# Optimization experiments

Measured on AMD Instinct MI355X. Metric: run time of the kernel, lower is better.

Reference implementation:

```python
import jax, jax.numpy as jnp
import numpy as np

N, E = 50000, 800000
IN_C, HID, OUT_C = 100, 128, 40
LAYERS, GROUPS, CODES = 3, 3, 16
BETA = 0.98
EPS = 1e-5


def setup_inputs() -> dict:
    key = jax.random.key(0)
    ks = jax.random.split(key, 16)
    lin = lambda k, i, o: (jax.random.normal(k, (i, o), jnp.float32) / np.sqrt(i)).astype(jnp.float32)
    d = {}
    d["x"] = jax.random.normal(ks[0], (N, IN_C), jnp.float32)
    d["src"] = jax.random.randint(ks[1], (E,), 0, N, jnp.int32)
    d["dst"] = jax.random.randint(ks[2], (E,), 0, N, jnp.int32)
    # SAGEConv params: lin_l (aggregated, with bias) and lin_r (root, no bias)
    d["W0a"], d["W0r"], d["b0"] = lin(ks[3], IN_C, HID), lin(ks[4], IN_C, HID), jnp.zeros((HID,), jnp.float32)
    d["W1a"], d["W1r"], d["b1"] = lin(ks[5], HID, HID), lin(ks[6], HID, HID), jnp.zeros((HID,), jnp.float32)
    d["W2a"], d["W2r"], d["b2"] = lin(ks[7], HID, HID), lin(ks[8], HID, HID), jnp.zeros((HID,), jnp.float32)
    # BatchNorm (eval mode: running stats) for first num_layers-1 = 2 layers
    d["bn_gamma"] = jnp.ones((2, HID), jnp.float32)
    d["bn_beta"] = jnp.zeros((2, HID), jnp.float32)
    d["bn_mean"] = jnp.zeros((2, HID), jnp.float32)
    d["bn_var"] = jnp.ones((2, HID), jnp.float32)
    # Residual VQ codebooks: [layer, group, num_codes, feature]
    d["codebooks"] = 0.1 * jax.random.normal(ks[9], (LAYERS, GROUPS, CODES, HID), jnp.float32)
    d["lin_W"] = lin(ks[10], HID, OUT_C)
    d["lin_b"] = jnp.zeros((OUT_C,), jnp.float32)
    return d


def _sage_conv(h, src, dst, Wa, Wr, b):
    # mean neighbor aggregation (PyG SAGEConv, aggr='mean')
    msg = h[src]                                              # [E, d]
    agg = jax.ops.segment_sum(msg, dst, num_segments=N)       # [N, d]
    deg = jax.ops.segment_sum(jnp.ones((E,), h.dtype), dst, num_segments=N)
    agg = agg / jnp.maximum(deg, 1.0)[:, None]
    return agg @ Wa + b + h @ Wr


def _rvq(h, cb):
    # residual vector quantization over GROUPS codebooks; cb: [G, K, D]
    res, quant, ids = h, jnp.zeros_like(h), []
    for g in range(GROUPS):
        c = cb[g]                                             # [K, D]
        d2 = (jnp.sum(res * res, -1, keepdims=True)
              - 2.0 * res @ c.T + jnp.sum(c * c, -1))          # [N, K]
        idx = jnp.argmin(d2, axis=-1)
        q = c[idx]
        quant = quant + q
        res = res - q
        ids.append(idx)
    sg = jax.lax.stop_gradient
    loss = (BETA * jnp.mean((h - sg(quant)) ** 2)
            + (1.0 - BETA) * jnp.mean((sg(h) - quant) ** 2))
    return loss, jnp.stack(ids, axis=1)                        # [N, G] int


def reference(x, src, dst, W0a, W0r, b0, W1a, W1r, b1, W2a, W2r, b2,
              bn_gamma, bn_beta, bn_mean, bn_var, codebooks, lin_W, lin_b):
    Ws = [(W0a, W0r, b0), (W1a, W1r, b1), (W2a, W2r, b2)]
    h = x
    total_loss = jnp.float32(0.0)
    id_list = []
    for i in range(LAYERS - 1):
        h = _sage_conv(h, src, dst, *Ws[i])
        h = (h - bn_mean[i]) * jax.lax.rsqrt(bn_var[i] + EPS) * bn_gamma[i] + bn_beta[i]
        h = jax.nn.relu(h)                                     # dropout: eval mode (identity)
        loss, ids = _rvq(h, codebooks[i])
        total_loss = total_loss + loss
        id_list.append(ids)
    h = _sage_conv(h, src, dst, *Ws[-1])
    loss, ids = _rvq(h, codebooks[-1])
    total_loss = total_loss + loss
    id_list.append(ids)
    out = h @ lin_W + lin_b
    return out, total_loss, jnp.concatenate(id_list, axis=1)
```

## Files before the change

### kernel.cpp

```cpp
#include <hip/hip_runtime.h>

#define NN 50000
#define HID 128
#define IN_C 100
#define OUT_C 40

__global__ __launch_bounds__(256)
void hist_kernel(const int* __restrict__ dst, int* __restrict__ deg, int E) {
    int e = blockIdx.x * 256 + threadIdx.x;
    if (e < E) atomicAdd(&deg[dst[e]], 1);
}

__global__ __launch_bounds__(256)
void chunk_sum_kernel(const int* __restrict__ deg, int* __restrict__ chunk_sums, int N) {
    __shared__ int s[256];
    const int t = threadIdx.x;
    const int i = blockIdx.x * 256 + t;
    s[t] = (i < N) ? deg[i] : 0;
    __syncthreads();
    for (int o = 128; o; o >>= 1) { if (t < o) s[t] += s[t + o]; __syncthreads(); }
    if (t == 0) chunk_sums[blockIdx.x] = s[0];
}

__global__ __launch_bounds__(256)
void chunk_scan_kernel(int* __restrict__ chunk_sums, int M) {
    __shared__ int s[256];
    const int t = threadIdx.x;
    int v = (t < M) ? chunk_sums[t] : 0;
    s[t] = v;
    __syncthreads();
    for (int o = 1; o < 256; o <<= 1) {
        int x = (t >= o) ? s[t - o] : 0;
        __syncthreads();
        s[t] += x;
        __syncthreads();
    }
    if (t < M) chunk_sums[t] = s[t] - v;
}

__global__ __launch_bounds__(256)
void chunk_apply_kernel(const int* __restrict__ deg, const int* __restrict__ chunk_sums,
                        int* __restrict__ row_start, int* __restrict__ cursor, int N) {
    __shared__ int s[256];
    const int t = threadIdx.x;
    const int i = blockIdx.x * 256 + t;
    int v = (i < N) ? deg[i] : 0;
    s[t] = v;
    __syncthreads();
    for (int o = 1; o < 256; o <<= 1) {
        int x = (t >= o) ? s[t - o] : 0;
        __syncthreads();
        s[t] += x;
        __syncthreads();
    }
    if (i < N) {
        int ex = chunk_sums[blockIdx.x] + s[t] - v;
        row_start[i] = ex;
        cursor[i] = ex;
        if (i == N - 1) row_start[N] = ex + v;
    }
}

__global__ __launch_bounds__(256)
void scatter_kernel(const int* __restrict__ src, const int* __restrict__ dst,
                    int* __restrict__ cursor, int* __restrict__ csr_src, int E) {
    int e = blockIdx.x * 256 + threadIdx.x;
    if (e < E) {
        int pos = atomicAdd(&cursor[dst[e]], 1);
        csr_src[pos] = src[e];
    }
}

__device__ __forceinline__ double2 ld2(const double* p) {
    return *(const double2*)p;
}
__device__ __forceinline__ double2 ld2(const float* p) {
    float2 v = *(const float2*)p;
    return make_double2((double)v.x, (double)v.y);
}

template<int K, bool HAS_BN, bool LAST, typename TIN>
__global__ __launch_bounds__(512, 6)
void layer_fused(const TIN* __restrict__ h_in,
                 const int* __restrict__ row_start, const int* __restrict__ csr_src,
                 const float* __restrict__ Wa, const float* __restrict__ Wr,
                 const float* __restrict__ b,
                 const float* __restrict__ gamma, const float* __restrict__ beta,
                 const float* __restrict__ mean, const float* __restrict__ var,
                 const float* __restrict__ cb,
                 double* __restrict__ h_out,
                 float* __restrict__ ids_out, int id_col0,
                 double* __restrict__ loss_part,
                 const float* __restrict__ lin_W, const float* __restrict__ lin_b,
                 float* __restrict__ out) {
    __shared__ double s_agg[8][HID];
    __shared__ double s_h[8][HID];
    __shared__ float s_cb[3 * 16 * HID];
    const int t = threadIdx.x;
    const int w = t >> 6, lane = t & 63;
    const int n0 = blockIdx.x * 8;

    for (int idx = t; idx < 3 * 16 * HID; idx += 512) s_cb[idx] = cb[idx];

    {
        const int n = n0 + w;
        const int r0 = row_start[n], r1 = row_start[n + 1];
        const int f0 = 2 * lane;
        if (f0 < K) {
            double s0 = 0, s1 = 0, s2 = 0, s3 = 0, s4 = 0, s5 = 0, s6 = 0, s7 = 0;
            int i = r0;
            for (; i + 3 < r1; i += 4) {
                double2 v0 = ld2(h_in + (size_t)csr_src[i] * K + f0);
                double2 v1 = ld2(h_in + (size_t)csr_src[i + 1] * K + f0);
                double2 v2 = ld2(h_in + (size_t)csr_src[i + 2] * K + f0);
                double2 v3 = ld2(h_in + (size_t)csr_src[i + 3] * K + f0);
                s0 += v0.x; s1 += v0.y; s2 += v1.x; s3 += v1.y;
                s4 += v2.x; s5 += v2.y; s6 += v3.x; s7 += v3.y;
            }
            for (; i < r1; ++i) {
                double2 v = ld2(h_in + (size_t)csr_src[i] * K + f0);
                s0 += v.x; s1 += v.y;
            }
            const int deg = r1 - r0;
            const double dd = (double)(deg > 1 ? deg : 1);
            const double2 root = ld2(h_in + (size_t)n * K + f0);
            s_agg[w][f0]     = ((s0 + s2) + (s4 + s6)) / dd;
            s_agg[w][f0 + 1] = ((s1 + s3) + (s5 + s7)) / dd;
            s_h[w][f0]     = root.x;
            s_h[w][f0 + 1] = root.y;
        }
    }
    __syncthreads();

    const int col = t & 127;
    const int p4 = t >> 7;
    double accA = (double)b[col];
    double accB = accA;
#pragma unroll 4
    for (int k = 0; k < K; ++k) {
        const double wa = (double)Wa[(size_t)k * HID + col];
        const double wr = (double)Wr[(size_t)k * HID + col];
        accA += s_agg[p4][k] * wa + s_h[p4][k] * wr;
        accB += s_agg[p4 + 4][k] * wa + s_h[p4 + 4][k] * wr;
    }
    __syncthreads();

    {
        double vA = accA, vB = accB;
        if (HAS_BN) {
            const double scale = (double)gamma[col] / sqrt((double)var[col] + 1e-5);
            const double shift = (double)beta[col] - (double)mean[col] * scale;
            vA = vA * scale + shift; vA = vA > 0.0 ? vA : 0.0;
            vB = vB * scale + shift; vB = vB > 0.0 ? vB : 0.0;
        }
        h_out[(size_t)(n0 + p4) * HID + col] = vA;
        h_out[(size_t)(n0 + p4 + 4) * HID + col] = vB;
        s_agg[p4][col] = vA;
        s_agg[p4 + 4][col] = vB;
        if (LAST) {
            s_h[p4][col] = vA;
            s_h[p4 + 4][col] = vB;
        }
    }
    __syncthreads();

    double wl;
    {
        double* res = &s_agg[w][0];
        const int n = n0 + w;
        const int k = lane & 15, q = lane >> 4;
        const int jbase = q * 32;
        const int rot = (k + 8 * q) & 31;

        for (int g = 0; g < 3; ++g) {
            const float* c = &s_cb[(g * 16 + k) * HID];
            double r0 = res[lane], r1 = res[lane + 64];
            double pr = r0 * r0 + r1 * r1;
            pr += __shfl_xor(pr, 1, 64);
            pr += __shfl_xor(pr, 2, 64);
            pr += __shfl_xor(pr, 4, 64);
            pr += __shfl_xor(pr, 8, 64);
            pr += __shfl_xor(pr, 16, 64);
            pr += __shfl_xor(pr, 32, 64);
            const float rr32 = (float)pr;

            double cc = 0.0, dot = 0.0;
#pragma unroll
            for (int j2 = 0; j2 < 32; ++j2) {
                const int j = jbase + ((j2 + rot) & 31);
                const double cj = (double)c[j];
                cc += cj * cj;
                dot += res[j] * cj;
            }
            cc += __shfl_xor(cc, 16, 64);
            cc += __shfl_xor(cc, 32, 64);
            dot += __shfl_xor(dot, 16, 64);
            dot += __shfl_xor(dot, 32, 64);

            const float cc32 = (float)cc;
            const float rc32 = (float)dot;
            const float t1 = rr32 - 2.0f * rc32;
            const float d2 = t1 + cc32;

            float bv = d2; int bk = k;
            {
                float ov; int ok;
                ov = __shfl_xor(bv, 1, 64); ok = __shfl_xor(bk, 1, 64);
                if (ov < bv || (ov == bv && ok < bk)) { bv = ov; bk = ok; }
                ov = __shfl_xor(bv, 2, 64); ok = __shfl_xor(bk, 2, 64);
                if (ov < bv || (ov == bv && ok < bk)) { bv = ov; bk = ok; }
                ov = __shfl_xor(bv, 4, 64); ok = __shfl_xor(bk, 4, 64);
                if (ov < bv || (ov == bv && ok < bk)) { bv = ov; bk = ok; }
                ov = __shfl_xor(bv, 8, 64); ok = __shfl_xor(bk, 8, 64);
                if (ov < bv || (ov == bv && ok < bk)) { bv = ov; bk = ok; }
            }
            if (lane == 0)
                ids_out[(size_t)n * 9 + id_col0 + g] = (float)bk;

            const float* cbest = &s_cb[(g * 16 + bk) * HID];
            res[lane]      -= (double)cbest[lane];
            res[lane + 64] -= (double)cbest[lane + 64];
        }
        double r0 = res[lane], r1 = res[lane + 64];
        wl = r0 * r0 + r1 * r1;
        wl += __shfl_xor(wl, 1, 64);
        wl += __shfl_xor(wl, 2, 64);
        wl += __shfl_xor(wl, 4, 64);
        wl += __shfl_xor(wl, 8, 64);
        wl += __shfl_xor(wl, 16, 64);
        wl += __shfl_xor(wl, 32, 64);
    }

    __syncthreads();
    if (lane == 0) s_agg[0][w] = wl;

    if (LAST) {
        const int n = n0 + w;
        if (lane < OUT_C) {
            double acc = (double)lin_b[lane];
            for (int kk = 0; kk < HID; ++kk)
                acc += s_h[w][kk] * (double)lin_W[kk * OUT_C + lane];
            out[(size_t)n * OUT_C + lane] = (float)acc;
        }
    }

    __syncthreads();
    if (t == 0) {
        double s = 0.0;
#pragma unroll
        for (int i = 0; i < 8; i++) s += s_agg[0][i];
        loss_part[blockIdx.x] = s;
    }
}

__global__ __launch_bounds__(256)
void finalize_kernel(const double* __restrict__ loss_part, int M,
                     float* __restrict__ out_loss) {
    __shared__ double s[256];
    const int t = threadIdx.x;
    double v = 0.0;
    for (int i = t; i < M; i += 256) v += loss_part[i];
    s[t] = v;
    __syncthreads();
    for (int off = 128; off; off >>= 1) {
        if (t < off) s[t] += s[t + off];
        __syncthreads();
    }
    if (t == 0) out_loss[0] = (float)(s[0] / ((double)NN * (double)HID));
}

extern "C" void kernel_launch(void* const* d_in, const int* in_sizes, int n_in,
                              void* d_out, int out_size, void* d_ws, size_t ws_size,
                              hipStream_t stream) {
    const float* x    = (const float*)d_in[0];
    const int*   src  = (const int*)d_in[1];
    const int*   dst  = (const int*)d_in[2];
    const float* W0a = (const float*)d_in[3];
    const float* W0r = (const float*)d_in[4];
    const float* b0  = (const float*)d_in[5];
    const float* W1a = (const float*)d_in[6];
    const float* W1r = (const float*)d_in[7];
    const float* b1  = (const float*)d_in[8];
    const float* W2a = (const float*)d_in[9];
    const float* W2r = (const float*)d_in[10];
    const float* b2  = (const float*)d_in[11];
    const float* bn_gamma = (const float*)d_in[12];
    const float* bn_beta  = (const float*)d_in[13];
    const float* bn_mean  = (const float*)d_in[14];
    const float* bn_var   = (const float*)d_in[15];
    const float* cb    = (const float*)d_in[16];
    const float* lin_W = (const float*)d_in[17];
    const float* lin_b = (const float*)d_in[18];

    const int E = in_sizes[1];

    float* out      = (float*)d_out;
    float* out_loss = out + (size_t)NN * OUT_C;
    float* out_ids  = out_loss + 1;

    char* base = (char*)d_ws;
    size_t off = 0;
    auto alloc = [&](size_t bytes) -> void* {
        off = (off + 511) & ~(size_t)511;
        void* p = base + off;
        off += bytes;
        return p;
    };
    int* deg_i      = (int*)alloc((size_t)NN * 4);
    int* row_start  = (int*)alloc((size_t)(NN + 1) * 4);
    int* cursor     = (int*)alloc((size_t)NN * 4);
    int* csr_src    = (int*)alloc((size_t)E * 4);
    int* chunk_sums = (int*)alloc(256 * 4);
    double* loss_part = (double*)alloc((size_t)3 * 6250 * 8);
    double* h1 = (double*)alloc((size_t)NN * HID * 8);
    double* h2 = (double*)alloc((size_t)NN * HID * 8);

    const int cb_layer = 3 * 16 * HID;
    const int NB = NN / 8;
    const int NCHUNK = (NN + 255) / 256;

    hipMemsetAsync(deg_i, 0, NN * sizeof(int), stream);
    hist_kernel<<<(E + 255) / 256, 256, 0, stream>>>(dst, deg_i, E);
    chunk_sum_kernel<<<NCHUNK, 256, 0, stream>>>(deg_i, chunk_sums, NN);
    chunk_scan_kernel<<<1, 256, 0, stream>>>(chunk_sums, NCHUNK);
    chunk_apply_kernel<<<NCHUNK, 256, 0, stream>>>(deg_i, chunk_sums, row_start, cursor, NN);
    scatter_kernel<<<(E + 255) / 256, 256, 0, stream>>>(src, dst, cursor, csr_src, E);

    layer_fused<IN_C, true, false, float><<<NB, 512, 0, stream>>>(
        x, row_start, csr_src, W0a, W0r, b0, bn_gamma, bn_beta, bn_mean, bn_var,
        cb + 0 * cb_layer, h1, out_ids, 0, loss_part, nullptr, nullptr, nullptr);

    layer_fused<HID, true, false, double><<<NB, 512, 0, stream>>>(
        h1, row_start, csr_src, W1a, W1r, b1,
        bn_gamma + HID, bn_beta + HID, bn_mean + HID, bn_var + HID,
        cb + 1 * cb_layer, h2, out_ids, 3, loss_part + NB, nullptr, nullptr, nullptr);

    layer_fused<HID, false, true, double><<<NB, 512, 0, stream>>>(
        h2, row_start, csr_src, W2a, W2r, b2, nullptr, nullptr, nullptr, nullptr,
        cb + 2 * cb_layer, h1, out_ids, 6, loss_part + 2 * NB, lin_W, lin_b, out);

    finalize_kernel<<<1, 256, 0, stream>>>(loss_part, 3 * NB, out_loss);
}
```

Before: 1.132 ms.

## Pad codebook rows in LDS, precompute code norms, simplify gather loop

Codebook rows in shared memory are padded to 129 floats to avoid bank conflicts, and the squared norms of the codes are computed once per block into shared memory instead of per wave and group. The neighbor gather loop drops the vectorized double2/float2 loads and 4-way unroll, using scalar element loads with 2-way unroll. A __syncthreads is removed by writing per-wave loss sums into a dedicated shared array. The scalar loads and lower unroll may reduce memory-level parallelism in the dominant gather phase.

```diff
diff --git a/kernel.cpp b/kernel.cpp
--- a/kernel.cpp
+++ b/kernel.cpp
@@ -69,14 +69,6 @@
         int pos = atomicAdd(&cursor[dst[e]], 1);
         csr_src[pos] = src[e];
     }
-}
-
-__device__ __forceinline__ double2 ld2(const double* p) {
-    return *(const double2*)p;
-}
-__device__ __forceinline__ double2 ld2(const float* p) {
-    float2 v = *(const float2*)p;
-    return make_double2((double)v.x, (double)v.y);
 }
 
 template<int K, bool HAS_BN, bool LAST, typename TIN>
@@ -95,39 +87,40 @@
                  float* __restrict__ out) {
     __shared__ double s_agg[8][HID];
     __shared__ double s_h[8][HID];
-    __shared__ float s_cb[3 * 16 * HID];
+    __shared__ float s_cb[3 * 16 * 129];
+    __shared__ float s_cc32[3][16];
+    __shared__ double s_ws[8];
     const int t = threadIdx.x;
     const int w = t >> 6, lane = t & 63;
     const int n0 = blockIdx.x * 8;
 
-    for (int idx = t; idx < 3 * 16 * HID; idx += 512) s_cb[idx] = cb[idx];
+    for (int idx = t; idx < 3 * 16 * 128; idx += 512)
+        s_cb[(idx >> 7) * 129 + (idx & 127)] = cb[idx];
 
     {
         const int n = n0 + w;
         const int r0 = row_start[n], r1 = row_start[n + 1];
         const int f0 = 2 * lane;
         if (f0 < K) {
-            double s0 = 0, s1 = 0, s2 = 0, s3 = 0, s4 = 0, s5 = 0, s6 = 0, s7 = 0;
+            double a0 = 0.0, a1 = 0.0, c0 = 0.0, c1 = 0.0;
             int i = r0;
-            for (; i + 3 < r1; i += 4) {
-                double2 v0 = ld2(h_in + (size_t)csr_src[i] * K + f0);
-                double2 v1 = ld2(h_in + (size_t)csr_src[i + 1] * K + f0);
-                double2 v2 = ld2(h_in + (size_t)csr_src[i + 2] * K + f0);
-                double2 v3 = ld2(h_in + (size_t)csr_src[i + 3] * K + f0);
-                s0 += v0.x; s1 += v0.y; s2 += v1.x; s3 += v1.y;
-                s4 += v2.x; s5 += v2.y; s6 += v3.x; s7 += v3.y;
+            for (; i + 1 < r1; i += 2) {
+                const TIN* p0 = h_in + (size_t)csr_src[i] * K + f0;
+                const TIN* p1 = h_in + (size_t)csr_src[i + 1] * K + f0;
+                a0 += (double)p0[0]; a1 += (double)p0[1];
+                c0 += (double)p1[0]; c1 += (double)p1[1];
             }
-            for (; i < r1; ++i) {
-                double2 v = ld2(h_in + (size_t)csr_src[i] * K + f0);
-                s0 += v.x; s1 += v.y;
+            if (i < r1) {
+                const TIN* p0 = h_in + (size_t)csr_src[i] * K + f0;
+                a0 += (double)p0[0]; a1 += (double)p0[1];
             }
             const int deg = r1 - r0;
             const double dd = (double)(deg > 1 ? deg : 1);
-            const double2 root = ld2(h_in + (size_t)n * K + f0);
-            s_agg[w][f0]     = ((s0 + s2) + (s4 + s6)) / dd;
-            s_agg[w][f0 + 1] = ((s1 + s3) + (s5 + s7)) / dd;
-            s_h[w][f0]     = root.x;
-            s_h[w][f0 + 1] = root.y;
+            const TIN* pr = h_in + (size_t)n * K + f0;
+            s_agg[w][f0]     = (a0 + c0) / dd;
+            s_agg[w][f0 + 1] = (a1 + c1) / dd;
+            s_h[w][f0]     = (double)pr[0];
+            s_h[w][f0 + 1] = (double)pr[1];
         }
     }
     __syncthreads();
@@ -162,18 +155,20 @@
             s_h[p4 + 4][col] = vB;
         }
     }
-    __syncthreads();
-
-    double wl;
+    if (t < 48) {
+        const float* c = &s_cb[t * 129];
+        double s = 0.0;
+        for (int j = 0; j < 128; j++) { double cj = (double)c[j]; s += cj * cj; }
+        s_cc32[t >> 4][t & 15] = (float)s;
+    }
+    __syncthreads();
+
     {
         double* res = &s_agg[w][0];
         const int n = n0 + w;
         const int k = lane & 15, q = lane >> 4;
-        const int jbase = q * 32;
-        const int rot = (k + 8 * q) & 31;
 
         for (int g = 0; g < 3; ++g) {
-            const float* c = &s_cb[(g * 16 + k) * HID];
             double r0 = res[lane], r1 = res[lane + 64];
             double pr = r0 * r0 + r1 * r1;
             pr += __shfl_xor(pr, 1, 64);
@@ -184,23 +179,19 @@
             pr += __shfl_xor(pr, 32, 64);
             const float rr32 = (float)pr;
 
-            double cc = 0.0, dot = 0.0;
+            const float* c = &s_cb[(g * 16 + k) * 129];
+            double dot = 0.0;
 #pragma unroll
             for (int j2 = 0; j2 < 32; ++j2) {
-                const int j = jbase + ((j2 + rot) & 31);
-                const double cj = (double)c[j];
-                cc += cj * cj;
-                dot += res[j] * cj;
+                int j = q * 32 + ((j2 + q * 8) & 31);
+                dot += res[j] * (double)c[j];
             }
-            cc += __shfl_xor(cc, 16, 64);
-            cc += __shfl_xor(cc, 32, 64);
             dot += __shfl_xor(dot, 16, 64);
             dot += __shfl_xor(dot, 32, 64);
 
-            const float cc32 = (float)cc;
             const float rc32 = (float)dot;
             const float t1 = rr32 - 2.0f * rc32;
-            const float d2 = t1 + cc32;
+            const float d2 = t1 + s_cc32[g][k];
 
             float bv = d2; int bk = k;
             {
@@ -217,22 +208,19 @@
             if (lane == 0)
                 ids_out[(size_t)n * 9 + id_col0 + g] = (float)bk;
 
-            const float* cbest = &s_cb[(g * 16 + bk) * HID];
-            res[lane]      -= (double)cbest[lane];
-            res[lane + 64] -= (double)cbest[lane + 64];
+            res[lane]      -= (double)s_cb[(g * 16 + bk) * 129 + lane];
+            res[lane + 64] -= (double)s_cb[(g * 16 + bk) * 129 + lane + 64];
         }
         double r0 = res[lane], r1 = res[lane + 64];
-        wl = r0 * r0 + r1 * r1;
+        double wl = r0 * r0 + r1 * r1;
         wl += __shfl_xor(wl, 1, 64);
         wl += __shfl_xor(wl, 2, 64);
         wl += __shfl_xor(wl, 4, 64);
         wl += __shfl_xor(wl, 8, 64);
         wl += __shfl_xor(wl, 16, 64);
         wl += __shfl_xor(wl, 32, 64);
-    }
-
-    __syncthreads();
-    if (lane == 0) s_agg[0][w] = wl;
+        if (lane == 0) s_ws[w] = wl;
+    }
 
     if (LAST) {
         const int n = n0 + w;
@@ -248,7 +236,7 @@
     if (t == 0) {
         double s = 0.0;
 #pragma unroll
-        for (int i = 0; i < 8; i++) s += s_agg[0][i];
+        for (int i = 0; i < 8; i++) s += s_ws[i];
         loss_part[blockIdx.x] = s;
     }
 }
```

After: 992.7 us. -12.3%, faster.
